# Optimization experiments

Measured on AMD Instinct MI355X. Metric: run time of the kernel, lower is better.

Reference implementation:

```python
import jax, jax.numpy as jnp
import numpy as np

NUM_GROUPS = 8
EPS = 1e-5
QB = 128.0  # 2 ** (8 - 1), b = 8 activation bits


def setup_inputs() -> dict:
    key = jax.random.key(0)
    k1, k2, k3 = jax.random.split(key, 3)
    B, IN, OUT = 8192, 4096, 4096
    x = jax.random.normal(k1, (B, IN), jnp.float32)
    # emulates the int8 sign buffer (values in {-1, +1}) stored as float
    qw = jnp.sign(jax.random.normal(k2, (OUT, IN), jnp.float32))
    bias = jax.random.normal(k3, (OUT,), jnp.float32) * 0.02
    return {"x": x, "qw": qw, "bias": bias}


def _ste_sign(z):
    # straight-through estimator: sign in fwd, identity grad in bwd
    return jax.lax.stop_gradient(jnp.sign(z) - z) + z


def reference(x, qw, bias):
    g = NUM_GROUPS
    # dequantize_weights: global mean-abs scale over the sign buffer
    alpha = jnp.mean(jnp.abs(qw))
    w = qw * alpha                                  # [OUT, IN]
    OUT, IN = w.shape
    # binarize_weights_groupwise: groups along out_features rows
    wg = w.reshape(g, OUT // g, IN)
    alpha_g = jnp.mean(jnp.abs(wg), axis=(1, 2), keepdims=True)
    bw = _ste_sign(wg - alpha_g).reshape(OUT, IN)   # values in {-1, 0, +1}
    # linear
    out = x @ bw.T + bias                           # [B, OUT]
    # quantize_activations_groupwise: groups along batch dim, b=8
    B = out.shape[0]
    og = out.reshape(g, B // g, OUT)
    gamma_g = jnp.max(jnp.abs(og), axis=(1, 2), keepdims=True)
    q = jnp.clip(og * QB / (gamma_g + EPS), -QB + EPS, QB - EPS)
    return q.reshape(B, OUT)
```

## Files before the change

kernel.cpp:

```cpp
#include <hip/hip_runtime.h>
#include <hip/hip_bf16.h>
#include <stdint.h>

#define B_DIM   8192
#define IN_DIM  4096
#define OUT_DIM 4096
#define QB_V    128.0f
#define EPS_V   1e-5f

typedef __attribute__((ext_vector_type(4))) float  f32x4;
typedef __attribute__((ext_vector_type(8))) __bf16 bf16x8;
typedef __attribute__((ext_vector_type(4))) __bf16 bf16x4;

__device__ __forceinline__ void gload_lds16(const void* g, void* l) {
  void* gp = const_cast<void*>(g);
  __builtin_amdgcn_global_load_lds(
      (__attribute__((address_space(1))) void*)gp,
      (__attribute__((address_space(3))) void*)l, 16, 0, 0);
}

__device__ __forceinline__ __bf16 sgnb(float d) {
  return (__bf16)((d > 0.f) ? 1.f : (d < 0.f ? -1.f : 0.f));
}

__global__ void k_init(unsigned* ws) {
  int t = threadIdx.x;
  if (t < 16) ws[t] = 0u;
}

__global__ __launch_bounds__(256) void k_qw_sums(const float* __restrict__ qw,
                                                 float* __restrict__ sums) {
  __shared__ float red[4];
  const int t = threadIdx.x;
  const size_t base = (size_t)blockIdx.x * 4096;
  float s = 0.f;
#pragma unroll
  for (int j = 0; j < 4; ++j) {
    f32x4 v = *(const f32x4*)(qw + base + (size_t)j * 1024 + t * 4);
    s += fabsf(v.x) + fabsf(v.y) + fabsf(v.z) + fabsf(v.w);
  }
#pragma unroll
  for (int off = 32; off > 0; off >>= 1) s += __shfl_xor(s, off);
  if ((t & 63) == 0) red[t >> 6] = s;
  __syncthreads();
  if (t == 0) {
    float bs = red[0] + red[1] + red[2] + red[3];
    atomicAdd(sums + (blockIdx.x >> 9), bs);
  }
}

__global__ __launch_bounds__(256) void k_conv_bw(const float* __restrict__ qw,
                                                 const float* __restrict__ sums,
                                                 __bf16* __restrict__ bw) {
  const size_t i = ((size_t)blockIdx.x * 256 + threadIdx.x) * 4;
  const int g = (int)(i >> 21);
  const float mu = sums[g] * (1.0f / 2097152.0f);
  f32x4 v = *(const f32x4*)(qw + i);
  bf16x4 r;
  r.x = sgnb(v.x - mu);
  r.y = sgnb(v.y - mu);
  r.z = sgnb(v.z - mu);
  r.w = sgnb(v.w - mu);
  *(bf16x4*)(bw + i) = r;
}

__global__ __launch_bounds__(256) void k_conv_x(const float* __restrict__ x,
                                                __bf16* __restrict__ xb) {
  const size_t i = ((size_t)blockIdx.x * 256 + threadIdx.x) * 4;
  f32x4 v = *(const f32x4*)(x + i);
  bf16x4 r;
  r.x = (__bf16)v.x; r.y = (__bf16)v.y; r.z = (__bf16)v.z; r.w = (__bf16)v.w;
  *(bf16x4*)(xb + i) = r;
}

template <int AMODE>
__global__ __launch_bounds__(256) void k_gemm(
    const __bf16* __restrict__ xa, const float* __restrict__ xf,
    const __bf16* __restrict__ bwb, const float* __restrict__ qw,
    const float* __restrict__ sums, const float* __restrict__ bias,
    float* __restrict__ out, unsigned* __restrict__ gamma_bits) {
  __shared__ __bf16 As[128 * 64];
  __shared__ __bf16 Bs[128 * 64];
  const int t = threadIdx.x;
  const int lane = t & 63;
  const int wv = t >> 6;
  const int wr = wv >> 1, wc = wv & 1;
  const int fr = lane & 15, fq = lane >> 4;
  const int bid = blockIdx.x;
  const int bm = bid & 63, bn = bid >> 6;
  const int brow = bm << 7, bcol = bn << 7;

  f32x4 acc[4][4] = {};

  const int c0row = t >> 3;
  const int ccol = (t & 7) << 3;

  float muB = 0.f;
  if (AMODE == 2) muB = sums[bcol >> 9] * (1.0f / 2097152.0f);

  for (int kt = 0; kt < IN_DIM / 64; ++kt) {
    const int k0 = kt << 6;
    if (AMODE == 0) {
      __syncthreads();
#pragma unroll
      for (int it = 0; it < 4; ++it) {
        const int row = c0row + it * 32;
        gload_lds16(xa + (size_t)(brow + row) * IN_DIM + k0 + ccol,
                    As + (row << 6) + ccol);
        gload_lds16(bwb + (size_t)(bcol + row) * IN_DIM + k0 + ccol,
                    Bs + (row << 6) + ccol);
      }
      __syncthreads();
    } else if (AMODE == 1) {
      f32x4 a0[4], a1[4];
#pragma unroll
      for (int it = 0; it < 4; ++it) {
        const int row = c0row + it * 32;
        const float* p = xf + (size_t)(brow + row) * IN_DIM + k0 + ccol;
        a0[it] = *(const f32x4*)p;
        a1[it] = *(const f32x4*)(p + 4);
      }
      __syncthreads();
#pragma unroll
      for (int it = 0; it < 4; ++it) {
        const int row = c0row + it * 32;
        gload_lds16(bwb + (size_t)(bcol + row) * IN_DIM + k0 + ccol,
                    Bs + (row << 6) + ccol);
      }
#pragma unroll
      for (int it = 0; it < 4; ++it) {
        const int row = c0row + it * 32;
        bf16x8 w;
        w[0] = (__bf16)a0[it].x; w[1] = (__bf16)a0[it].y;
        w[2] = (__bf16)a0[it].z; w[3] = (__bf16)a0[it].w;
        w[4] = (__bf16)a1[it].x; w[5] = (__bf16)a1[it].y;
        w[6] = (__bf16)a1[it].z; w[7] = (__bf16)a1[it].w;
        *(bf16x8*)(As + (row << 6) + ccol) = w;
      }
      __syncthreads();
    } else {
      f32x4 a0[4], a1[4], b0[4], b1[4];
#pragma unroll
      for (int it = 0; it < 4; ++it) {
        const int row = c0row + it * 32;
        const float* pa = xf + (size_t)(brow + row) * IN_DIM + k0 + ccol;
        a0[it] = *(const f32x4*)pa;
        a1[it] = *(const f32x4*)(pa + 4);
        const float* pb = qw + (size_t)(bcol + row) * IN_DIM + k0 + ccol;
        b0[it] = *(const f32x4*)pb;
        b1[it] = *(const f32x4*)(pb + 4);
      }
      __syncthreads();
#pragma unroll
      for (int it = 0; it < 4; ++it) {
        const int row = c0row + it * 32;
        bf16x8 wa, wb;
        wa[0] = (__bf16)a0[it].x; wa[1] = (__bf16)a0[it].y;
        wa[2] = (__bf16)a0[it].z; wa[3] = (__bf16)a0[it].w;
        wa[4] = (__bf16)a1[it].x; wa[5] = (__bf16)a1[it].y;
        wa[6] = (__bf16)a1[it].z; wa[7] = (__bf16)a1[it].w;
        wb[0] = sgnb(b0[it].x - muB); wb[1] = sgnb(b0[it].y - muB);
        wb[2] = sgnb(b0[it].z - muB); wb[3] = sgnb(b0[it].w - muB);
        wb[4] = sgnb(b1[it].x - muB); wb[5] = sgnb(b1[it].y - muB);
        wb[6] = sgnb(b1[it].z - muB); wb[7] = sgnb(b1[it].w - muB);
        *(bf16x8*)(As + (row << 6) + ccol) = wa;
        *(bf16x8*)(Bs + (row << 6) + ccol) = wb;
      }
      __syncthreads();
    }

#pragma unroll
    for (int ks = 0; ks < 2; ++ks) {
      bf16x8 af[4], bfr[4];
#pragma unroll
      for (int mi = 0; mi < 4; ++mi)
        af[mi] = *(const bf16x8*)(As + ((wr << 6) + (mi << 4) + fr) * 64 +
                                  (ks << 5) + (fq << 3));
#pragma unroll
      for (int ni = 0; ni < 4; ++ni)
        bfr[ni] = *(const bf16x8*)(Bs + ((wc << 6) + (ni << 4) + fr) * 64 +
                                   (ks << 5) + (fq << 3));
#pragma unroll
      for (int mi = 0; mi < 4; ++mi)
#pragma unroll
        for (int ni = 0; ni < 4; ++ni)
          acc[mi][ni] = __builtin_amdgcn_mfma_f32_16x16x32_bf16(
              af[mi], bfr[ni], acc[mi][ni], 0, 0, 0);
    }
  }

  float mx = 0.f;
  const int colbase = bcol + (wc << 6);
#pragma unroll
  for (int ni = 0; ni < 4; ++ni) {
    const int col = colbase + (ni << 4) + fr;
    const float bv = bias[col];
#pragma unroll
    for (int mi = 0; mi < 4; ++mi) {
      const int rowb = brow + (wr << 6) + (mi << 4) + (fq << 2);
#pragma unroll
      for (int j = 0; j < 4; ++j) {
        const float v = acc[mi][ni][j] + bv;
        out[(size_t)(rowb + j) * OUT_DIM + col] = v;
        mx = fmaxf(mx, fabsf(v));
      }
    }
  }
#pragma unroll
  for (int off = 32; off > 0; off >>= 1) mx = fmaxf(mx, __shfl_xor(mx, off));
  if (lane == 0)
    atomicMax(gamma_bits + (brow >> 10), __float_as_uint(mx));
}

__global__ __launch_bounds__(256) void k_scale(float* __restrict__ out,
                                               const unsigned* __restrict__ gb) {
  const size_t i = ((size_t)blockIdx.x * 256 + threadIdx.x) * 4;
  const int g = (int)(i >> 22);
  const float gamma = __uint_as_float(gb[g]);
  const float sc = QB_V / (gamma + EPS_V);
  const float lo = -QB_V + EPS_V, hi = QB_V - EPS_V;
  f32x4 v = *(const f32x4*)(out + i);
  v.x = fminf(fmaxf(v.x * sc, lo), hi);
  v.y = fminf(fmaxf(v.y * sc, lo), hi);
  v.z = fminf(fmaxf(v.z * sc, lo), hi);
  v.w = fminf(fmaxf(v.w * sc, lo), hi);
  *(f32x4*)(out + i) = v;
}

extern "C" void kernel_launch(void* const* d_in, const int* in_sizes, int n_in,
                              void* d_out, int out_size, void* d_ws,
                              size_t ws_size, hipStream_t stream) {
  const float* x = (const float*)d_in[0];
  const float* qw = (const float*)d_in[1];
  const float* bias = (const float*)d_in[2];
  float* out = (float*)d_out;
  char* ws = (char*)d_ws;
  float* sums = (float*)ws;
  unsigned* gamma = (unsigned*)ws + 8;
  __bf16* bwb = (__bf16*)(ws + 256);
  __bf16* xb = (__bf16*)(ws + 256 + (size_t)OUT_DIM * IN_DIM * 2);

  const size_t need1 = 256 + (size_t)OUT_DIM * IN_DIM * 2;
  const size_t need0 = need1 + (size_t)B_DIM * IN_DIM * 2;
  const int amode = (ws_size >= need0) ? 0 : ((ws_size >= need1) ? 1 : 2);

  k_init<<<1, 64, 0, stream>>>((unsigned*)ws);
  k_qw_sums<<<4096, 256, 0, stream>>>(qw, sums);
  if (amode <= 1) k_conv_bw<<<16384, 256, 0, stream>>>(qw, sums, bwb);
  if (amode == 0) k_conv_x<<<32768, 256, 0, stream>>>(x, xb);

  if (amode == 0)
    k_gemm<0><<<2048, 256, 0, stream>>>(xb, x, bwb, qw, sums, bias, out, gamma);
  else if (amode == 1)
    k_gemm<1><<<2048, 256, 0, stream>>>(xb, x, bwb, qw, sums, bias, out, gamma);
  else
    k_gemm<2><<<2048, 256, 0, stream>>>(xb, x, bwb, qw, sums, bias, out, gamma);

  k_scale<<<32768, 256, 0, stream>>>(out, gamma);
}
```

Baseline: 807.6 us.

## Swizzle LDS tiles, remap GEMM block order, widen elementwise kernels

Applies an XOR swizzle to the 16-byte chunks of the A/B shared-memory tiles, permuting the global source columns so the linear LDS destination holds swizzled data, and reads the MFMA fragments with the matching XOR to avoid LDS bank conflicts. It also remaps block IDs so consecutive blocks spread across column tiles, which changes L2 reuse and how work lands across XCDs. The conversion and scale kernels now handle 16 elements per thread with fewer blocks. The swizzle must match exactly between writes and reads, and the block remap may help or hurt cache locality.

```diff
diff --git a/kernel.cpp b/kernel.cpp
--- a/kernel.cpp
+++ b/kernel.cpp
@@ -52,25 +52,36 @@
 __global__ __launch_bounds__(256) void k_conv_bw(const float* __restrict__ qw,
                                                  const float* __restrict__ sums,
                                                  __bf16* __restrict__ bw) {
-  const size_t i = ((size_t)blockIdx.x * 256 + threadIdx.x) * 4;
+  const size_t i = ((size_t)blockIdx.x * 256 + threadIdx.x) * 16;
   const int g = (int)(i >> 21);
   const float mu = sums[g] * (1.0f / 2097152.0f);
-  f32x4 v = *(const f32x4*)(qw + i);
-  bf16x4 r;
-  r.x = sgnb(v.x - mu);
-  r.y = sgnb(v.y - mu);
-  r.z = sgnb(v.z - mu);
-  r.w = sgnb(v.w - mu);
-  *(bf16x4*)(bw + i) = r;
+#pragma unroll
+  for (int h = 0; h < 2; ++h) {
+    f32x4 v0 = *(const f32x4*)(qw + i + h * 8);
+    f32x4 v1 = *(const f32x4*)(qw + i + h * 8 + 4);
+    bf16x8 r;
+    r[0] = sgnb(v0.x - mu); r[1] = sgnb(v0.y - mu);
+    r[2] = sgnb(v0.z - mu); r[3] = sgnb(v0.w - mu);
+    r[4] = sgnb(v1.x - mu); r[5] = sgnb(v1.y - mu);
+    r[6] = sgnb(v1.z - mu); r[7] = sgnb(v1.w - mu);
+    *(bf16x8*)(bw + i + h * 8) = r;
+  }
 }
 
 __global__ __launch_bounds__(256) void k_conv_x(const float* __restrict__ x,
                                                 __bf16* __restrict__ xb) {
-  const size_t i = ((size_t)blockIdx.x * 256 + threadIdx.x) * 4;
-  f32x4 v = *(const f32x4*)(x + i);
-  bf16x4 r;
-  r.x = (__bf16)v.x; r.y = (__bf16)v.y; r.z = (__bf16)v.z; r.w = (__bf16)v.w;
-  *(bf16x4*)(xb + i) = r;
+  const size_t i = ((size_t)blockIdx.x * 256 + threadIdx.x) * 16;
+#pragma unroll
+  for (int h = 0; h < 2; ++h) {
+    f32x4 v0 = *(const f32x4*)(x + i + h * 8);
+    f32x4 v1 = *(const f32x4*)(x + i + h * 8 + 4);
+    bf16x8 r;
+    r[0] = (__bf16)v0.x; r[1] = (__bf16)v0.y;
+    r[2] = (__bf16)v0.z; r[3] = (__bf16)v0.w;
+    r[4] = (__bf16)v1.x; r[5] = (__bf16)v1.y;
+    r[6] = (__bf16)v1.z; r[7] = (__bf16)v1.w;
+    *(bf16x8*)(xb + i + h * 8) = r;
+  }
 }
 
 template <int AMODE>
@@ -86,14 +97,19 @@
   const int wv = t >> 6;
   const int wr = wv >> 1, wc = wv & 1;
   const int fr = lane & 15, fq = lane >> 4;
-  const int bid = blockIdx.x;
+  const int fr7 = fr & 7;
+  const int orig = blockIdx.x;
+  const int bid = ((orig & 7) << 8) | (orig >> 3);
   const int bm = bid & 63, bn = bid >> 6;
   const int brow = bm << 7, bcol = bn << 7;
 
   f32x4 acc[4][4] = {};
 
   const int c0row = t >> 3;
-  const int ccol = (t & 7) << 3;
+  const int cchunk = t & 7;
+  const int schunk = cchunk ^ (c0row & 7);
+  const int ccol = cchunk << 3;
+  const int scol = schunk << 3;
 
   float muB = 0.f;
   if (AMODE == 2) muB = sums[bcol >> 9] * (1.0f / 2097152.0f);
@@ -105,9 +121,9 @@
 #pragma unroll
       for (int it = 0; it < 4; ++it) {
         const int row = c0row + it * 32;
-        gload_lds16(xa + (size_t)(brow + row) * IN_DIM + k0 + ccol,
+        gload_lds16(xa + (size_t)(brow + row) * IN_DIM + k0 + scol,
                     As + (row << 6) + ccol);
-        gload_lds16(bwb + (size_t)(bcol + row) * IN_DIM + k0 + ccol,
+        gload_lds16(bwb + (size_t)(bcol + row) * IN_DIM + k0 + scol,
                     Bs + (row << 6) + ccol);
       }
       __syncthreads();
@@ -116,7 +132,7 @@
 #pragma unroll
       for (int it = 0; it < 4; ++it) {
         const int row = c0row + it * 32;
-        const float* p = xf + (size_t)(brow + row) * IN_DIM + k0 + ccol;
+        const float* p = xf + (size_t)(brow + row) * IN_DIM + k0 + scol;
         a0[it] = *(const f32x4*)p;
         a1[it] = *(const f32x4*)(p + 4);
       }
@@ -124,7 +140,7 @@
 #pragma unroll
       for (int it = 0; it < 4; ++it) {
         const int row = c0row + it * 32;
-        gload_lds16(bwb + (size_t)(bcol + row) * IN_DIM + k0 + ccol,
+        gload_lds16(bwb + (size_t)(bcol + row) * IN_DIM + k0 + scol,
                     Bs + (row << 6) + ccol);
       }
 #pragma unroll
@@ -143,10 +159,10 @@
 #pragma unroll
       for (int it = 0; it < 4; ++it) {
         const int row = c0row + it * 32;
-        const float* pa = xf + (size_t)(brow + row) * IN_DIM + k0 + ccol;
+        const float* pa = xf + (size_t)(brow + row) * IN_DIM + k0 + scol;
         a0[it] = *(const f32x4*)pa;
         a1[it] = *(const f32x4*)(pa + 4);
-        const float* pb = qw + (size_t)(bcol + row) * IN_DIM + k0 + ccol;
+        const float* pb = qw + (size_t)(bcol + row) * IN_DIM + k0 + scol;
         b0[it] = *(const f32x4*)pb;
         b1[it] = *(const f32x4*)(pb + 4);
       }
@@ -174,12 +190,12 @@
       bf16x8 af[4], bfr[4];
 #pragma unroll
       for (int mi = 0; mi < 4; ++mi)
-        af[mi] = *(const bf16x8*)(As + ((wr << 6) + (mi << 4) + fr) * 64 +
-                                  (ks << 5) + (fq << 3));
+        af[mi] = *(const bf16x8*)(As + (((wr << 6) + (mi << 4) + fr) << 6) +
+                                  ((((ks << 2) | fq) ^ fr7) << 3));
 #pragma unroll
       for (int ni = 0; ni < 4; ++ni)
-        bfr[ni] = *(const bf16x8*)(Bs + ((wc << 6) + (ni << 4) + fr) * 64 +
-                                   (ks << 5) + (fq << 3));
+        bfr[ni] = *(const bf16x8*)(Bs + (((wc << 6) + (ni << 4) + fr) << 6) +
+                                   ((((ks << 2) | fq) ^ fr7) << 3));
 #pragma unroll
       for (int mi = 0; mi < 4; ++mi)
 #pragma unroll
@@ -214,17 +230,20 @@
 
 __global__ __launch_bounds__(256) void k_scale(float* __restrict__ out,
                                                const unsigned* __restrict__ gb) {
-  const size_t i = ((size_t)blockIdx.x * 256 + threadIdx.x) * 4;
+  const size_t i = ((size_t)blockIdx.x * 256 + threadIdx.x) * 16;
   const int g = (int)(i >> 22);
   const float gamma = __uint_as_float(gb[g]);
   const float sc = QB_V / (gamma + EPS_V);
   const float lo = -QB_V + EPS_V, hi = QB_V - EPS_V;
-  f32x4 v = *(const f32x4*)(out + i);
-  v.x = fminf(fmaxf(v.x * sc, lo), hi);
-  v.y = fminf(fmaxf(v.y * sc, lo), hi);
-  v.z = fminf(fmaxf(v.z * sc, lo), hi);
-  v.w = fminf(fmaxf(v.w * sc, lo), hi);
-  *(f32x4*)(out + i) = v;
+#pragma unroll
+  for (int h = 0; h < 4; ++h) {
+    f32x4 v = *(const f32x4*)(out + i + h * 4);
+    v.x = fminf(fmaxf(v.x * sc, lo), hi);
+    v.y = fminf(fmaxf(v.y * sc, lo), hi);
+    v.z = fminf(fmaxf(v.z * sc, lo), hi);
+    v.w = fminf(fmaxf(v.w * sc, lo), hi);
+    *(f32x4*)(out + i + h * 4) = v;
+  }
 }
 
 extern "C" void kernel_launch(void* const* d_in, const int* in_sizes, int n_in,
@@ -246,8 +265,8 @@
 
   k_init<<<1, 64, 0, stream>>>((unsigned*)ws);
   k_qw_sums<<<4096, 256, 0, stream>>>(qw, sums);
-  if (amode <= 1) k_conv_bw<<<16384, 256, 0, stream>>>(qw, sums, bwb);
-  if (amode == 0) k_conv_x<<<32768, 256, 0, stream>>>(x, xb);
+  if (amode <= 1) k_conv_bw<<<4096, 256, 0, stream>>>(qw, sums, bwb);
+  if (amode == 0) k_conv_x<<<8192, 256, 0, stream>>>(x, xb);
 
   if (amode == 0)
     k_gemm<0><<<2048, 256, 0, stream>>>(xb, x, bwb, qw, sums, bias, out, gamma);
@@ -256,5 +275,5 @@
   else
     k_gemm<2><<<2048, 256, 0, stream>>>(xb, x, bwb, qw, sums, bias, out, gamma);
 
-  k_scale<<<32768, 256, 0, stream>>>(out, gamma);
-}
+  k_scale<<<8192, 256, 0, stream>>>(out, gamma);
+}
```

Measured after the change: 819.5 us. Within noise of the previous version (+1.5%).
